# Optimization experiments

Hardware: AMD Instinct MI355X
Metric: run time of the kernel (lower is better)

## Reference

```python
import jax, jax.numpy as jnp
import numpy as np

N, C_IN, C_OUT, T, V, K = 32, 64, 128, 300, 25, 3
EPS = 1e-5


def setup_inputs() -> dict:
    key = jax.random.key(0)
    ks = jax.random.split(key, 10)
    x = jax.random.normal(ks[0], (N, C_IN, T, V), dtype=jnp.float32)
    # fixed adjacency buffer (requires_grad=False in torch) and learned attention mask
    A = jax.random.uniform(ks[1], (K, V, V), dtype=jnp.float32)
    graph_attn = jnp.ones((K, V, V), dtype=jnp.float32)  # nn.init.constant_(1)
    # per-subset 1x1 conv weights/biases, stacked: [K, C_out, C_in]
    Wg = jax.random.normal(ks[2], (K, C_OUT, C_IN), dtype=jnp.float32) * np.sqrt(2.0 / (C_OUT * K))
    bg = jnp.zeros((K, C_OUT), dtype=jnp.float32)
    # main BN affine (torch init: weight=1e-6, bias=0; use small random for a nontrivial test)
    bn_gamma = jax.random.normal(ks[3], (C_OUT,), dtype=jnp.float32) * 0.1 + 1.0
    bn_beta = jax.random.normal(ks[4], (C_OUT,), dtype=jnp.float32) * 0.1
    # residual branch (in != out): 1x1 conv + BN
    Wr = jax.random.normal(ks[5], (C_OUT, C_IN), dtype=jnp.float32) * np.sqrt(2.0 / C_IN)
    br = jnp.zeros((C_OUT,), dtype=jnp.float32)
    rbn_gamma = jax.random.normal(ks[6], (C_OUT,), dtype=jnp.float32) * 0.1 + 1.0
    rbn_beta = jax.random.normal(ks[7], (C_OUT,), dtype=jnp.float32) * 0.1
    return {"x": x, "A": A, "graph_attn": graph_attn, "Wg": Wg, "bg": bg,
            "bn_gamma": bn_gamma, "bn_beta": bn_beta,
            "Wr": Wr, "br": br, "rbn_gamma": rbn_gamma, "rbn_beta": rbn_beta}


def _batchnorm(z, gamma, beta):
    # training-mode BatchNorm2d: biased batch stats over (N, T, V)
    mean = jnp.mean(z, axis=(0, 2, 3), keepdims=True)
    var = jnp.var(z, axis=(0, 2, 3), keepdims=True)
    zhat = (z - mean) * jax.lax.rsqrt(var + EPS)
    return zhat * gamma[None, :, None, None] + beta[None, :, None, None]


def reference(x, A, graph_attn, Wg, bg, bn_gamma, bn_beta, Wr, br, rbn_gamma, rbn_beta):
    Ae = A * graph_attn                                   # [K, V, V]
    # per-subset graph aggregation: (x.view(N, C*T, V) @ Ae[k])  -> [K, N, C, T, V]
    xA = jnp.einsum('nctv,kvw->knctw', x, Ae)
    # per-subset 1x1 conv then sum over subsets; biases sum as well
    hidden = jnp.einsum('knctv,koc->notv', xA, Wg) + jnp.sum(bg, axis=0)[None, :, None, None]
    hidden = _batchnorm(hidden, bn_gamma, bn_beta)
    # residual: 1x1 conv + BN (since in_channels != out_channels)
    res = jnp.einsum('nctv,oc->notv', x, Wr) + br[None, :, None, None]
    res = _batchnorm(res, rbn_gamma, rbn_beta)
    return hidden + res
```

## Files before the change

kernel.cpp:

```cpp
#include <hip/hip_runtime.h>

typedef __attribute__((ext_vector_type(8))) _Float16 half8;
typedef __attribute__((ext_vector_type(4))) _Float16 half4v;
typedef __attribute__((ext_vector_type(4))) float float4v;
typedef __attribute__((ext_vector_type(4))) unsigned int uint4v;
typedef float float4u __attribute__((ext_vector_type(4), aligned(4)));
typedef unsigned long long u64;
typedef unsigned int u32;

#define NB   32
#define CIN  64
#define COUT 128
#define TT   300
#define VV   25
#define EPS  1e-5f
#define M_TOT 240000.0f
#define NBLK 1600
#define NTILE 4800

#define WS_WF    0
#define WS_AEF   65536
#define WS_ST    73728
#define WS_CF    75776
#define WS_WF2   77312
#define WS_TRASH 143360
#define WS_HR    1048576
#define WS_PARTP (WS_HR + 137625600)
#define WS_NEED  (WS_PARTP + 3276800)

__device__ __forceinline__ void bar_lds() {
    __builtin_amdgcn_sched_barrier(0);
    asm volatile("s_waitcnt lgkmcnt(0)" ::: "memory");
    __builtin_amdgcn_s_barrier();
    __builtin_amdgcn_sched_barrier(0);
}

__device__ __forceinline__ unsigned short f2h(float f) {
    return __builtin_bit_cast(unsigned short, (_Float16)f);
}
__device__ __forceinline__ float4v mfma16(half8 a, half8 b, float4v c) {
    return __builtin_amdgcn_mfma_f32_16x16x32_f16(a, b, c, 0, 0, 0);
}
__device__ __forceinline__ u32 pk2(float a, float b) {
    return __builtin_bit_cast(u32, __builtin_amdgcn_cvt_pkrtz(a, b));
}
__device__ __forceinline__ int hr_off(int cm, int on) {
    return (cm & 1) ? (2048 + (cm >> 1) * 768 + on * 384)
                    : ((cm >> 1) * 1024 + on * 512);
}

__global__ void prep_kernel(const float* __restrict__ A, const float* __restrict__ ga,
                            const float* __restrict__ Wg, const float* __restrict__ Wr,
                            char* __restrict__ wsb) {
    unsigned short* wf = (unsigned short*)(wsb + WS_WF);
    unsigned short* ae = (unsigned short*)(wsb + WS_AEF);
    float* st = (float*)(wsb + WS_ST);
    int i = blockIdx.x * blockDim.x + threadIdx.x;
    for (; i < 32768 + 4096 + 512; i += gridDim.x * blockDim.x) {
        if (i < 32768) {
            int on = i >> 12, kt = (i >> 9) & 7, l = (i >> 3) & 63, j = i & 7;
            int o = on * 16 + (l & 15);
            int kc = kt * 32 + ((l >> 4) << 3) + j;
            float v = (kc < 192) ? Wg[((kc >> 6) * COUT + o) * CIN + (kc & 63)]
                                 : Wr[o * CIN + (kc - 192)];
            wf[i] = f2h(v);
        } else if (i < 32768 + 4096) {
            int q = i - 32768;
            int k = q >> 10, nt = (q >> 9) & 1, l = (q >> 3) & 63, j = q & 7;
            int v = ((l >> 4) << 3) + j, w = nt * 16 + (l & 15);
            float val = 0.0f;
            if (v < VV && w < VV)
                val = (k < 3) ? A[(k * VV + v) * VV + w] * ga[(k * VV + v) * VV + w]
                              : (v == w ? 1.0f : 0.0f);
            ae[q] = f2h(val);
        } else {
            st[i - 36864] = 0.0f;
        }
    }
}

__global__ __launch_bounds__(256) void red_kernel(const float* __restrict__ part,
                                                  char* __restrict__ wsb) {
    float* st = (float*)(wsb + WS_ST);
    __shared__ float red[4][4];
    const int tid = threadIdx.x, wv = tid >> 6, lane = tid & 63;
    const int i0 = blockIdx.x * 4;
    const int bi = tid >> 2, ii = tid & 3;
    float s = 0.0f;
    for (int b = bi; b < NBLK; b += 64)
        s += part[(size_t)b * 512 + i0 + ii];
    s += __shfl_xor(s, 4);
    s += __shfl_xor(s, 8);
    s += __shfl_xor(s, 16);
    s += __shfl_xor(s, 32);
    if (lane < 4) red[wv][lane] = s;
    __syncthreads();
    if (tid < 4) st[i0 + tid] = red[0][tid] + red[1][tid] + red[2][tid] + red[3][tid];
}

__global__ __launch_bounds__(256) void scale_kernel(
        const float* __restrict__ Wg, const float* __restrict__ Wr,
        const float* __restrict__ g1, const float* __restrict__ b1,
        const float* __restrict__ g2, const float* __restrict__ b2,
        char* __restrict__ wsb, int fillw2) {
    const float* st = (const float*)(wsb + WS_ST);
    float* cf = (float*)(wsb + WS_CF);
    unsigned short* wf2 = (unsigned short*)(wsb + WS_WF2);
    __shared__ float cl[384];
    int tid = threadIdx.x;
    if (tid < 128) {
        int o = tid;
        const float inv_m = 1.0f / M_TOT;
        float mH = st[o] * inv_m,        vH = st[128 + o] * inv_m - mH * mH;
        float mR = st[256 + o] * inv_m,  vR = st[384 + o] * inv_m - mR * mR;
        float scH = g1[o] * rsqrtf(vH + EPS);
        float scR = g2[o] * rsqrtf(vR + EPS);
        float bC  = b1[o] + b2[o] - scH * mH - scR * mR;
        cl[o] = scH; cl[128 + o] = scR; cl[256 + o] = bC;
        if (blockIdx.x == 0) { cf[o] = scH; cf[128 + o] = scR; cf[256 + o] = bC; }
    }
    __syncthreads();
    if (!fillw2) return;
    for (int i = blockIdx.x * 256 + tid; i < 32768; i += gridDim.x * 256) {
        int on = i >> 12, kt = (i >> 9) & 7, l = (i >> 3) & 63, j = i & 7;
        int o = on * 16 + (l & 15);
        int kc = kt * 32 + ((l >> 4) << 3) + j;
        float v = (kc < 192) ? Wg[((kc >> 6) * COUT + o) * CIN + (kc & 63)] * cl[o]
                             : Wr[o * CIN + (kc - 192)] * cl[128 + o];
        wf2[i] = f2h(v);
    }
}

template <int MODE>
__global__ __launch_bounds__(256, 2) void gcn_kernel(
        const float* __restrict__ x, char* __restrict__ wsb, float* __restrict__ out,
        float* __restrict__ part) {
    __shared__ __align__(16) _Float16 xa[64 * 256];
    char* xab = (char*)xa;

    const unsigned short* wf = (const unsigned short*)(wsb + (MODE == 1 ? WS_WF2 : WS_WF));
    const unsigned short* ae = (const unsigned short*)(wsb + WS_AEF);
    const float* cf = (const float*)(wsb + WS_CF);

    const int tid = threadIdx.x, wv = tid >> 6, l = tid & 63;
    const int l15 = l & 15, lq = l >> 4;

    half8 af[2][8];
#pragma unroll
    for (int on = 0; on < 2; ++on)
#pragma unroll
        for (int kt = 0; kt < 8; ++kt)
            af[on][kt] = *(const half8*)&wf[(((wv * 2 + on) * 8 + kt) * 64 + l) * 8];

    half8 aef[4][2];
#pragma unroll
    for (int k = 0; k < 4; ++k)
#pragma unroll
        for (int nt = 0; nt < 2; ++nt)
            aef[k][nt] = *(const half8*)&ae[((k * 2 + nt) * 64 + l) * 8];

    float bC2[2];
    if (MODE == 1) {
#pragma unroll
        for (int on = 0; on < 2; ++on)
            bC2[on] = cf[256 + wv * 32 + on * 16 + l15];
    }

    float sH[2], sH2[2], sR[2], sR2[2];
    if (MODE != 1) {
#pragma unroll
        for (int on = 0; on < 2; ++on) { sH[on] = 0; sH2[on] = 0; sR[on] = 0; sR2[on] = 0; }
    }

    const int cRow = wv * 16 + l15;
    const int va = (lq * 8 > 16) ? 16 : lq * 8;
    float4u A1[2], A2[2];
    float Bv[2];
    auto ld_tile = [&](int n_, int t0_) {
#pragma unroll
        for (int t = 0; t < 2; ++t) {
            const float* base = x + n_ * 480000 + cRow * 7500 + (t0_ + t) * 25;
            A1[t] = *(const float4u*)(base + va);
            A2[t] = *(const float4u*)(base + va + 4);
            Bv[t] = base[24];
        }
    };
    auto mk_xf = [&](int t) -> half8 {
        u32 w0 = pk2(A1[t][0], A1[t][1]), w1 = pk2(A1[t][2], A1[t][3]);
        u32 w2 = pk2(A2[t][0], A2[t][1]), w3 = pk2(A2[t][2], A2[t][3]);
        if (lq == 3) { w0 = pk2(Bv[t], 0.0f); w1 = 0; w2 = 0; w3 = 0; }
        uint4v uw = {w0, w1, w2, w3};
        return __builtin_bit_cast(half8, uw);
    };

    const int swb = (blockIdx.x & 7) * (NBLK / 8) + (blockIdx.x >> 3);
    const int tile0 = swb * 3;
    ld_tile(tile0 / 150, (tile0 % 150) * 2);

    for (int it = 0; it < 3; ++it) {
        const int tile = tile0 + it;
        const int n = tile / 150, t0 = (tile % 150) * 2;
        bar_lds();

        half8 xf0 = mk_xf(0);
        half8 xf1 = mk_xf(1);
        if (it < 2) { int tl = tile + 1; ld_tile(tl / 150, (tl % 150) * 2); }

        {
            half8 xfs[2] = {xf0, xf1};
#pragma unroll
            for (int t = 0; t < 2; ++t)
#pragma unroll
                for (int k = 0; k < 4; ++k)
#pragma unroll
                    for (int nt = 0; nt < 2; ++nt) {
                        float4v c4 = {0.0f, 0.0f, 0.0f, 0.0f};
                        c4 = mfma16(xfs[t], aef[k][nt], c4);
                        int col = t * 32 + nt * 16 + l15;
                        int kcb = (k * 64 + wv * 16 + lq * 4) * 2;
                        u64 pk = ((u64)pk2(c4[2], c4[3]) << 32) | pk2(c4[0], c4[1]);
                        *(u64*)(xab + ((col << 9) + (kcb ^ ((col & 7) << 4)))) = pk;
                    }
        }
        bar_lds();

        char* hrw = wsb + WS_HR + (size_t)tile * 28672 + wv * 7168;

        float4v acc[4][2];
        if (MODE != 1) {
#pragma unroll
            for (int cm = 0; cm < 4; ++cm)
#pragma unroll
                for (int on = 0; on < 2; ++on) acc[cm][on] = {0.0f, 0.0f, 0.0f, 0.0f};
            __builtin_amdgcn_s_setprio(1);
#pragma unroll
            for (int kt = 0; kt < 6; ++kt)
#pragma unroll
                for (int cm = 0; cm < 4; ++cm) {
                    int col = cm * 16 + l15;
                    half8 bf = *(const half8*)(xab + ((col << 9) +
                                   ((kt * 64 + lq * 16) ^ ((col & 7) << 4))));
                    acc[cm][0] = mfma16(bf, af[0][kt], acc[cm][0]);
                    acc[cm][1] = mfma16(bf, af[1][kt], acc[cm][1]);
                }
            __builtin_amdgcn_s_setprio(0);
#pragma unroll
            for (int cm = 0; cm < 4; ++cm)
#pragma unroll
                for (int on = 0; on < 2; ++on) {
#pragma unroll
                    for (int r = 0; r < 4; ++r) {
                        float h = acc[cm][on][r];
                        sH[on] += h; sH2[on] += h * h;
                    }
                    if (MODE == 2) {
                        u64 p = (u64)pk2(acc[cm][on][0], acc[cm][on][1]) |
                                ((u64)pk2(acc[cm][on][2], acc[cm][on][3]) << 32);
                        char* dst = hrw + hr_off(cm, on) + l * 8;
                        if ((cm & 1) && lq == 3) dst = wsb + WS_TRASH;
                        *(u64*)dst = p;
                    }
                    acc[cm][on] = {0.0f, 0.0f, 0.0f, 0.0f};
                }
            __builtin_amdgcn_s_setprio(1);
#pragma unroll
            for (int kt = 6; kt < 8; ++kt)
#pragma unroll
                for (int cm = 0; cm < 4; ++cm) {
                    int col = cm * 16 + l15;
                    half8 bf = *(const half8*)(xab + ((col << 9) +
                                   ((kt * 64 + lq * 16) ^ ((col & 7) << 4))));
                    acc[cm][0] = mfma16(bf, af[0][kt], acc[cm][0]);
                    acc[cm][1] = mfma16(bf, af[1][kt], acc[cm][1]);
                }
            __builtin_amdgcn_s_setprio(0);
#pragma unroll
            for (int cm = 0; cm < 4; ++cm)
#pragma unroll
                for (int on = 0; on < 2; ++on) {
#pragma unroll
                    for (int r = 0; r < 4; ++r) {
                        float rv = acc[cm][on][r];
                        sR[on] += rv; sR2[on] += rv * rv;
                    }
                    if (MODE == 2) {
                        u64 p = (u64)pk2(acc[cm][on][0], acc[cm][on][1]) |
                                ((u64)pk2(acc[cm][on][2], acc[cm][on][3]) << 32);
                        char* dst = hrw + 3584 + hr_off(cm, on) + l * 8;
                        if ((cm & 1) && lq == 3) dst = wsb + WS_TRASH;
                        *(u64*)dst = p;
                    }
                }
        } else {
#pragma unroll
            for (int cm = 0; cm < 4; ++cm)
#pragma unroll
                for (int on = 0; on < 2; ++on)
#pragma unroll
                    for (int r = 0; r < 4; ++r) acc[cm][on][r] = bC2[on];
            __builtin_amdgcn_s_setprio(1);
#pragma unroll
            for (int kt = 0; kt < 8; ++kt)
#pragma unroll
                for (int cm = 0; cm < 4; ++cm) {
                    int col = cm * 16 + l15;
                    half8 bf = *(const half8*)(xab + ((col << 9) +
                                   ((kt * 64 + lq * 16) ^ ((col & 7) << 4))));
                    acc[cm][0] = mfma16(bf, af[0][kt], acc[cm][0]);
                    acc[cm][1] = mfma16(bf, af[1][kt], acc[cm][1]);
                }
            __builtin_amdgcn_s_setprio(0);
#pragma unroll
            for (int cm = 0; cm < 4; ++cm) {
                int t = t0 + (cm >> 1);
#pragma unroll
                for (int on = 0; on < 2; ++on) {
                    int o = wv * 32 + on * 16 + l15;
                    float* op = out + ((size_t)(n * COUT + o) * TT + t) * VV;
                    if (!(cm & 1)) {
                        *(float4u*)(op + lq * 4) = acc[cm][on];
                    } else if (lq < 2) {
                        *(float4u*)(op + 16 + lq * 4) = acc[cm][on];
                    } else if (lq == 2) {
                        op[24] = acc[cm][on][0];
                    }
                }
            }
        }
    }

    if (MODE != 1) {
#pragma unroll
        for (int on = 0; on < 2; ++on) {
            sH[on]  += __shfl_xor(sH[on], 16);  sH[on]  += __shfl_xor(sH[on], 32);
            sH2[on] += __shfl_xor(sH2[on], 16); sH2[on] += __shfl_xor(sH2[on], 32);
            sR[on]  += __shfl_xor(sR[on], 16);  sR[on]  += __shfl_xor(sR[on], 32);
            sR2[on] += __shfl_xor(sR2[on], 16); sR2[on] += __shfl_xor(sR2[on], 32);
        }
        if (l < 16) {
            float* pb = part + (size_t)blockIdx.x * 512;
#pragma unroll
            for (int on = 0; on < 2; ++on) {
                int o = wv * 32 + on * 16 + l15;
                pb[o]       = sH[on];
                pb[128 + o] = sH2[on];
                pb[256 + o] = sR[on];
                pb[384 + o] = sR2[on];
            }
        }
    }
}

__global__ __launch_bounds__(256) void bn_apply(const char* __restrict__ wsb,
                                                float* __restrict__ out) {
    __shared__ u64 lds[3584];
    const float* cf = (const float*)(wsb + WS_CF);
    const int tile = blockIdx.x;
    const int n = tile / 150, t0 = (tile % 150) * 2;
    const int tid = threadIdx.x;

    const u64* src = (const u64*)(wsb + WS_HR + (size_t)tile * 28672);
#pragma unroll
    for (int i = 0; i < 14; ++i) lds[tid + i * 256] = src[tid + i * 256];
    __syncthreads();

#pragma unroll
    for (int i = 0; i < 7; ++i) {
        int j2 = tid + i * 256;
        int row = j2 / 7, q = j2 - row * 7;
        int o = row >> 1, t = row & 1;
        int v0 = (q < 6) ? q * 4 : 24;
        int cm = t * 2 + (v0 >> 4);
        int lq = (v0 & 15) >> 2;
        int ll = lq * 16 + (o & 15);
        int wv = o >> 5, on = (o >> 4) & 1;
        int offq = (cm & 1) ? (256 + (cm >> 1) * 96 + on * 48)
                            : ((cm >> 1) * 128 + on * 64);
        u64 h64 = lds[wv * 896 + offq + ll];
        u64 r64 = lds[wv * 896 + 448 + offq + ll];
        half4v h4 = __builtin_bit_cast(half4v, h64);
        half4v r4 = __builtin_bit_cast(half4v, r64);
        float scH = cf[o], scR = cf[128 + o], bC = cf[256 + o];
        float* op = out + ((size_t)(n * COUT + o) * TT + t0 + t) * VV + v0;
        if (q < 6) {
            float4u v;
#pragma unroll
            for (int k = 0; k < 4; ++k)
                v[k] = scH * (float)h4[k] + scR * (float)r4[k] + bC;
            *(float4u*)op = v;
        } else {
            op[0] = scH * (float)h4[0] + scR * (float)r4[0] + bC;
        }
    }
}

extern "C" void kernel_launch(void* const* d_in, const int* in_sizes, int n_in,
                              void* d_out, int out_size, void* d_ws, size_t ws_size,
                              hipStream_t stream) {
    const float* x        = (const float*)d_in[0];
    const float* A        = (const float*)d_in[1];
    const float* ga       = (const float*)d_in[2];
    const float* Wg       = (const float*)d_in[3];
    const float* bn_gamma = (const float*)d_in[5];
    const float* bn_beta  = (const float*)d_in[6];
    const float* Wr       = (const float*)d_in[7];
    const float* rbn_g    = (const float*)d_in[9];
    const float* rbn_b    = (const float*)d_in[10];
    char* wsb  = (char*)d_ws;
    float* out = (float*)d_out;

    const bool primary = ws_size >= (size_t)WS_NEED + 4096;
    float* partP = (float*)(wsb + WS_PARTP);
    float* partF = (float*)(wsb + WS_HR);

    prep_kernel<<<64, 256, 0, stream>>>(A, ga, Wg, Wr, wsb);
    if (primary) {
        gcn_kernel<2><<<NBLK, 256, 0, stream>>>(x, wsb, nullptr, partP);
        red_kernel<<<128, 256, 0, stream>>>(partP, wsb);
        scale_kernel<<<64, 256, 0, stream>>>(Wg, Wr, bn_gamma, bn_beta, rbn_g, rbn_b, wsb, 0);
        bn_apply<<<NTILE, 256, 0, stream>>>(wsb, out);
    } else {
        gcn_kernel<0><<<NBLK, 256, 0, stream>>>(x, wsb, nullptr, partF);
        red_kernel<<<128, 256, 0, stream>>>(partF, wsb);
        scale_kernel<<<64, 256, 0, stream>>>(Wg, Wr, bn_gamma, bn_beta, rbn_g, rbn_b, wsb, 1);
        gcn_kernel<1><<<NBLK, 256, 0, stream>>>(x, wsb, out, partF);
    }
}
```

Before: 131.2 us.

## Double-buffer LDS stage-1 tile to overlap with stage-2 MFMA

Doubles the LDS buffer so the graph-aggregation MFMA for the next tile writes into the alternate buffer while the current tile's 1x1-conv MFMA reads the other one. This removes one barrier per iteration and lets stage 1 and stage 2 interleave. It also drops the separate scalar tail load by reading an overlapping float4 at offset 21, removes the s_setprio hints, and fully unrolls the 3-iteration loop. The cost is doubled LDS (64KB per block), which may limit occupancy at 2 blocks/CU, plus more registers for the two staged input sets.

```diff
diff --git a/kernel.cpp b/kernel.cpp
--- a/kernel.cpp
+++ b/kernel.cpp
@@ -135,7 +135,7 @@
 __global__ __launch_bounds__(256, 2) void gcn_kernel(
         const float* __restrict__ x, char* __restrict__ wsb, float* __restrict__ out,
         float* __restrict__ part) {
-    __shared__ __align__(16) _Float16 xa[64 * 256];
+    __shared__ __align__(16) _Float16 xa[2][64 * 256];
     char* xab = (char*)xa;
 
     const unsigned short* wf = (const unsigned short*)(wsb + (MODE == 1 ? WS_WF2 : WS_WF));
@@ -173,57 +173,63 @@
     }
 
     const int cRow = wv * 16 + l15;
-    const int va = (lq * 8 > 16) ? 16 : lq * 8;
-    float4u A1[2], A2[2];
-    float Bv[2];
-    auto ld_tile = [&](int n_, int t0_) {
+    const int va1 = (lq >= 2) ? 16 : lq * 8;
+    const int va2 = (lq == 3) ? 21 : va1 + 4;
+    float4u A1[2][2], A2[2][2];
+
+    auto ld_tile = [&](int s, int tl) {
+        int n_ = tl / 150, t0_ = (tl % 150) * 2;
 #pragma unroll
         for (int t = 0; t < 2; ++t) {
             const float* base = x + n_ * 480000 + cRow * 7500 + (t0_ + t) * 25;
-            A1[t] = *(const float4u*)(base + va);
-            A2[t] = *(const float4u*)(base + va + 4);
-            Bv[t] = base[24];
+            A1[s][t] = *(const float4u*)(base + va1);
+            A2[s][t] = *(const float4u*)(base + va2);
         }
     };
-    auto mk_xf = [&](int t) -> half8 {
-        u32 w0 = pk2(A1[t][0], A1[t][1]), w1 = pk2(A1[t][2], A1[t][3]);
-        u32 w2 = pk2(A2[t][0], A2[t][1]), w3 = pk2(A2[t][2], A2[t][3]);
-        if (lq == 3) { w0 = pk2(Bv[t], 0.0f); w1 = 0; w2 = 0; w3 = 0; }
+    auto mk_xf = [&](int s, int t) -> half8 {
+        u32 w0 = pk2(A1[s][t][0], A1[s][t][1]), w1 = pk2(A1[s][t][2], A1[s][t][3]);
+        u32 w2 = pk2(A2[s][t][0], A2[s][t][1]), w3 = pk2(A2[s][t][2], A2[s][t][3]);
+        if (lq == 3) { w0 = pk2(A2[s][t][3], 0.0f); w1 = 0; w2 = 0; w3 = 0; }
         uint4v uw = {w0, w1, w2, w3};
         return __builtin_bit_cast(half8, uw);
     };
+    auto do_stage1 = [&](int s, int buf) {
+        char* xb = xab + buf * 32768;
+#pragma unroll
+        for (int t = 0; t < 2; ++t) {
+            half8 xf = mk_xf(s, t);
+#pragma unroll
+            for (int k = 0; k < 4; ++k)
+#pragma unroll
+                for (int nt = 0; nt < 2; ++nt) {
+                    float4v c4 = {0.0f, 0.0f, 0.0f, 0.0f};
+                    c4 = mfma16(xf, aef[k][nt], c4);
+                    int col = t * 32 + nt * 16 + l15;
+                    int kcb = (k * 64 + wv * 16 + lq * 4) * 2;
+                    u64 pk = ((u64)pk2(c4[2], c4[3]) << 32) | pk2(c4[0], c4[1]);
+                    *(u64*)(xb + ((col << 9) + (kcb ^ ((col & 7) << 4)))) = pk;
+                }
+        }
+    };
 
     const int swb = (blockIdx.x & 7) * (NBLK / 8) + (blockIdx.x >> 3);
     const int tile0 = swb * 3;
-    ld_tile(tile0 / 150, (tile0 % 150) * 2);
-
+
+    ld_tile(0, tile0);
+    do_stage1(0, 0);
+    ld_tile(1, tile0 + 1);
+
+#pragma unroll
     for (int it = 0; it < 3; ++it) {
         const int tile = tile0 + it;
         const int n = tile / 150, t0 = (tile % 150) * 2;
+        const int buf = it & 1;
         bar_lds();
 
-        half8 xf0 = mk_xf(0);
-        half8 xf1 = mk_xf(1);
-        if (it < 2) { int tl = tile + 1; ld_tile(tl / 150, (tl % 150) * 2); }
-
-        {
-            half8 xfs[2] = {xf0, xf1};
-#pragma unroll
-            for (int t = 0; t < 2; ++t)
-#pragma unroll
-                for (int k = 0; k < 4; ++k)
-#pragma unroll
-                    for (int nt = 0; nt < 2; ++nt) {
-                        float4v c4 = {0.0f, 0.0f, 0.0f, 0.0f};
-                        c4 = mfma16(xfs[t], aef[k][nt], c4);
-                        int col = t * 32 + nt * 16 + l15;
-                        int kcb = (k * 64 + wv * 16 + lq * 4) * 2;
-                        u64 pk = ((u64)pk2(c4[2], c4[3]) << 32) | pk2(c4[0], c4[1]);
-                        *(u64*)(xab + ((col << 9) + (kcb ^ ((col & 7) << 4)))) = pk;
-                    }
-        }
-        bar_lds();
-
+        if (it == 0) ld_tile(0, tile0 + 2);
+        if (it < 2) do_stage1((it + 1) & 1, (it + 1) & 1);
+
+        char* xb = xab + buf * 32768;
         char* hrw = wsb + WS_HR + (size_t)tile * 28672 + wv * 7168;
 
         float4v acc[4][2];
@@ -232,18 +238,16 @@
             for (int cm = 0; cm < 4; ++cm)
 #pragma unroll
                 for (int on = 0; on < 2; ++on) acc[cm][on] = {0.0f, 0.0f, 0.0f, 0.0f};
-            __builtin_amdgcn_s_setprio(1);
 #pragma unroll
             for (int kt = 0; kt < 6; ++kt)
 #pragma unroll
                 for (int cm = 0; cm < 4; ++cm) {
                     int col = cm * 16 + l15;
-                    half8 bf = *(const half8*)(xab + ((col << 9) +
+                    half8 bf = *(const half8*)(xb + ((col << 9) +
                                    ((kt * 64 + lq * 16) ^ ((col & 7) << 4))));
                     acc[cm][0] = mfma16(bf, af[0][kt], acc[cm][0]);
                     acc[cm][1] = mfma16(bf, af[1][kt], acc[cm][1]);
                 }
-            __builtin_amdgcn_s_setprio(0);
 #pragma unroll
             for (int cm = 0; cm < 4; ++cm)
 #pragma unroll
@@ -262,18 +266,16 @@
                     }
                     acc[cm][on] = {0.0f, 0.0f, 0.0f, 0.0f};
                 }
-            __builtin_amdgcn_s_setprio(1);
 #pragma unroll
             for (int kt = 6; kt < 8; ++kt)
 #pragma unroll
                 for (int cm = 0; cm < 4; ++cm) {
                     int col = cm * 16 + l15;
-                    half8 bf = *(const half8*)(xab + ((col << 9) +
+                    half8 bf = *(const half8*)(xb + ((col << 9) +
                                    ((kt * 64 + lq * 16) ^ ((col & 7) << 4))));
                     acc[cm][0] = mfma16(bf, af[0][kt], acc[cm][0]);
                     acc[cm][1] = mfma16(bf, af[1][kt], acc[cm][1]);
                 }
-            __builtin_amdgcn_s_setprio(0);
 #pragma unroll
             for (int cm = 0; cm < 4; ++cm)
 #pragma unroll
@@ -298,18 +300,16 @@
                 for (int on = 0; on < 2; ++on)
 #pragma unroll
                     for (int r = 0; r < 4; ++r) acc[cm][on][r] = bC2[on];
-            __builtin_amdgcn_s_setprio(1);
 #pragma unroll
             for (int kt = 0; kt < 8; ++kt)
 #pragma unroll
                 for (int cm = 0; cm < 4; ++cm) {
                     int col = cm * 16 + l15;
-                    half8 bf = *(const half8*)(xab + ((col << 9) +
+                    half8 bf = *(const half8*)(xb + ((col << 9) +
                                    ((kt * 64 + lq * 16) ^ ((col & 7) << 4))));
                     acc[cm][0] = mfma16(bf, af[0][kt], acc[cm][0]);
                     acc[cm][1] = mfma16(bf, af[1][kt], acc[cm][1]);
                 }
-            __builtin_amdgcn_s_setprio(0);
 #pragma unroll
             for (int cm = 0; cm < 4; ++cm) {
                 int t = t0 + (cm >> 1);
```

New measurement: 123.1 us. -6.2%, faster.

## Split gcn_kernel work across 8 waves with 512-thread blocks

Applied to the files above, without the earlier changes.

Doubles the block size of gcn_kernel from 256 to 512 threads, so each wave now handles one 16-row output group instead of two, and one time step of the graph aggregation instead of two. Per-thread register arrays (weight fragments, accumulators, BN partial sums) are halved. The aim is more waves in flight to hide memory and LDS latency, and lower register pressure per thread. In exchange, each weight/B fragment loaded from LDS is reused by half as many MFMAs, and launch bounds now demand 4 blocks of 512 threads per CU.

```diff
diff --git a/kernel.cpp b/kernel.cpp
--- a/kernel.cpp
+++ b/kernel.cpp
@@ -58,8 +58,8 @@
     int i = blockIdx.x * blockDim.x + threadIdx.x;
     for (; i < 32768 + 4096 + 512; i += gridDim.x * blockDim.x) {
         if (i < 32768) {
-            int on = i >> 12, kt = (i >> 9) & 7, l = (i >> 3) & 63, j = i & 7;
-            int o = on * 16 + (l & 15);
+            int og = i >> 12, kt = (i >> 9) & 7, l = (i >> 3) & 63, j = i & 7;
+            int o = og * 16 + (l & 15);
             int kc = kt * 32 + ((l >> 4) << 3) + j;
             float v = (kc < 192) ? Wg[((kc >> 6) * COUT + o) * CIN + (kc & 63)]
                                  : Wr[o * CIN + (kc - 192)];
@@ -122,8 +122,8 @@
     __syncthreads();
     if (!fillw2) return;
     for (int i = blockIdx.x * 256 + tid; i < 32768; i += gridDim.x * 256) {
-        int on = i >> 12, kt = (i >> 9) & 7, l = (i >> 3) & 63, j = i & 7;
-        int o = on * 16 + (l & 15);
+        int og = i >> 12, kt = (i >> 9) & 7, l = (i >> 3) & 63, j = i & 7;
+        int o = og * 16 + (l & 15);
         int kc = kt * 32 + ((l >> 4) << 3) + j;
         float v = (kc < 192) ? Wg[((kc >> 6) * COUT + o) * CIN + (kc & 63)] * cl[o]
                              : Wr[o * CIN + (kc - 192)] * cl[128 + o];
@@ -132,7 +132,7 @@
 }
 
 template <int MODE>
-__global__ __launch_bounds__(256, 2) void gcn_kernel(
+__global__ __launch_bounds__(512, 4) void gcn_kernel(
         const float* __restrict__ x, char* __restrict__ wsb, float* __restrict__ out,
         float* __restrict__ part) {
     __shared__ __align__(16) _Float16 xa[64 * 256];
@@ -142,15 +142,14 @@
     const unsigned short* ae = (const unsigned short*)(wsb + WS_AEF);
     const float* cf = (const float*)(wsb + WS_CF);
 
-    const int tid = threadIdx.x, wv = tid >> 6, l = tid & 63;
+    const int tid = threadIdx.x, w = tid >> 6, l = tid & 63;
     const int l15 = l & 15, lq = l >> 4;
-
-    half8 af[2][8];
-#pragma unroll
-    for (int on = 0; on < 2; ++on)
-#pragma unroll
-        for (int kt = 0; kt < 8; ++kt)
-            af[on][kt] = *(const half8*)&wf[(((wv * 2 + on) * 8 + kt) * 64 + l) * 8];
+    const int wv4 = w & 3, tloc = w >> 2;
+
+    half8 af[8];
+#pragma unroll
+    for (int kt = 0; kt < 8; ++kt)
+        af[kt] = *(const half8*)&wf[((w * 8 + kt) * 64 + l) * 8];
 
     half8 aef[4][2];
 #pragma unroll
@@ -159,79 +158,62 @@
         for (int nt = 0; nt < 2; ++nt)
             aef[k][nt] = *(const half8*)&ae[((k * 2 + nt) * 64 + l) * 8];
 
-    float bC2[2];
-    if (MODE == 1) {
-#pragma unroll
-        for (int on = 0; on < 2; ++on)
-            bC2[on] = cf[256 + wv * 32 + on * 16 + l15];
-    }
-
-    float sH[2], sH2[2], sR[2], sR2[2];
-    if (MODE != 1) {
-#pragma unroll
-        for (int on = 0; on < 2; ++on) { sH[on] = 0; sH2[on] = 0; sR[on] = 0; sR2[on] = 0; }
-    }
-
-    const int cRow = wv * 16 + l15;
+    float bC2;
+    if (MODE == 1) bC2 = cf[256 + w * 16 + l15];
+
+    float sH = 0, sH2 = 0, sR = 0, sR2 = 0;
+
+    const int cRow = wv4 * 16 + l15;
     const int va = (lq * 8 > 16) ? 16 : lq * 8;
-    float4u A1[2], A2[2];
-    float Bv[2];
-    auto ld_tile = [&](int n_, int t0_) {
-#pragma unroll
-        for (int t = 0; t < 2; ++t) {
-            const float* base = x + n_ * 480000 + cRow * 7500 + (t0_ + t) * 25;
-            A1[t] = *(const float4u*)(base + va);
-            A2[t] = *(const float4u*)(base + va + 4);
-            Bv[t] = base[24];
-        }
+    float4u A1, A2;
+    float Bv;
+    auto ld_tile = [&](int tl) {
+        int n_ = tl / 150, t0_ = (tl % 150) * 2;
+        const float* base = x + n_ * 480000 + cRow * 7500 + (t0_ + tloc) * 25;
+        A1 = *(const float4u*)(base + va);
+        A2 = *(const float4u*)(base + va + 4);
+        Bv = base[24];
     };
-    auto mk_xf = [&](int t) -> half8 {
-        u32 w0 = pk2(A1[t][0], A1[t][1]), w1 = pk2(A1[t][2], A1[t][3]);
-        u32 w2 = pk2(A2[t][0], A2[t][1]), w3 = pk2(A2[t][2], A2[t][3]);
-        if (lq == 3) { w0 = pk2(Bv[t], 0.0f); w1 = 0; w2 = 0; w3 = 0; }
+    auto mk_xf = [&]() -> half8 {
+        u32 w0 = pk2(A1[0], A1[1]), w1 = pk2(A1[2], A1[3]);
+        u32 w2 = pk2(A2[0], A2[1]), w3 = pk2(A2[2], A2[3]);
+        if (lq == 3) { w0 = pk2(Bv, 0.0f); w1 = 0; w2 = 0; w3 = 0; }
         uint4v uw = {w0, w1, w2, w3};
         return __builtin_bit_cast(half8, uw);
     };
 
     const int swb = (blockIdx.x & 7) * (NBLK / 8) + (blockIdx.x >> 3);
     const int tile0 = swb * 3;
-    ld_tile(tile0 / 150, (tile0 % 150) * 2);
+    ld_tile(tile0);
 
     for (int it = 0; it < 3; ++it) {
         const int tile = tile0 + it;
         const int n = tile / 150, t0 = (tile % 150) * 2;
         bar_lds();
 
-        half8 xf0 = mk_xf(0);
-        half8 xf1 = mk_xf(1);
-        if (it < 2) { int tl = tile + 1; ld_tile(tl / 150, (tl % 150) * 2); }
-
-        {
-            half8 xfs[2] = {xf0, xf1};
-#pragma unroll
-            for (int t = 0; t < 2; ++t)
-#pragma unroll
-                for (int k = 0; k < 4; ++k)
-#pragma unroll
-                    for (int nt = 0; nt < 2; ++nt) {
-                        float4v c4 = {0.0f, 0.0f, 0.0f, 0.0f};
-                        c4 = mfma16(xfs[t], aef[k][nt], c4);
-                        int col = t * 32 + nt * 16 + l15;
-                        int kcb = (k * 64 + wv * 16 + lq * 4) * 2;
-                        u64 pk = ((u64)pk2(c4[2], c4[3]) << 32) | pk2(c4[0], c4[1]);
-                        *(u64*)(xab + ((col << 9) + (kcb ^ ((col & 7) << 4)))) = pk;
-                    }
-        }
+        half8 xf = mk_xf();
+        if (it < 2) ld_tile(tile + 1);
+
+#pragma unroll
+        for (int k = 0; k < 4; ++k)
+#pragma unroll
+            for (int nt = 0; nt < 2; ++nt) {
+                float4v c4 = {0.0f, 0.0f, 0.0f, 0.0f};
+                c4 = mfma16(xf, aef[k][nt], c4);
+                int col = tloc * 32 + nt * 16 + l15;
+                int kcb = (k * 64 + wv4 * 16 + lq * 4) * 2;
+                u64 pk = ((u64)pk2(c4[2], c4[3]) << 32) | pk2(c4[0], c4[1]);
+                *(u64*)(xab + ((col << 9) + (kcb ^ ((col & 7) << 4)))) = pk;
+            }
         bar_lds();
 
-        char* hrw = wsb + WS_HR + (size_t)tile * 28672 + wv * 7168;
-
-        float4v acc[4][2];
+        char* hrw = wsb + WS_HR + (size_t)tile * 28672 + (w >> 1) * 7168;
+        const int on = w & 1;
+
+        float4v acc[4];
         if (MODE != 1) {
 #pragma unroll
-            for (int cm = 0; cm < 4; ++cm)
-#pragma unroll
-                for (int on = 0; on < 2; ++on) acc[cm][on] = {0.0f, 0.0f, 0.0f, 0.0f};
+            for (int cm = 0; cm < 4; ++cm) acc[cm] = {0.0f, 0.0f, 0.0f, 0.0f};
             __builtin_amdgcn_s_setprio(1);
 #pragma unroll
             for (int kt = 0; kt < 6; ++kt)
@@ -240,28 +222,25 @@
                     int col = cm * 16 + l15;
                     half8 bf = *(const half8*)(xab + ((col << 9) +
                                    ((kt * 64 + lq * 16) ^ ((col & 7) << 4))));
-                    acc[cm][0] = mfma16(bf, af[0][kt], acc[cm][0]);
-                    acc[cm][1] = mfma16(bf, af[1][kt], acc[cm][1]);
+                    acc[cm] = mfma16(bf, af[kt], acc[cm]);
                 }
             __builtin_amdgcn_s_setprio(0);
 #pragma unroll
-            for (int cm = 0; cm < 4; ++cm)
-#pragma unroll
-                for (int on = 0; on < 2; ++on) {
-#pragma unroll
-                    for (int r = 0; r < 4; ++r) {
-                        float h = acc[cm][on][r];
-                        sH[on] += h; sH2[on] += h * h;
-                    }
-                    if (MODE == 2) {
-                        u64 p = (u64)pk2(acc[cm][on][0], acc[cm][on][1]) |
-                                ((u64)pk2(acc[cm][on][2], acc[cm][on][3]) << 32);
-                        char* dst = hrw + hr_off(cm, on) + l * 8;
-                        if ((cm & 1) && lq == 3) dst = wsb + WS_TRASH;
-                        *(u64*)dst = p;
-                    }
-                    acc[cm][on] = {0.0f, 0.0f, 0.0f, 0.0f};
-                }
+            for (int cm = 0; cm < 4; ++cm) {
+#pragma unroll
+                for (int r = 0; r < 4; ++r) {
+                    float h = acc[cm][r];
+                    sH += h; sH2 += h * h;
+                }
+                if (MODE == 2) {
+                    u64 p = (u64)pk2(acc[cm][0], acc[cm][1]) |
+                            ((u64)pk2(acc[cm][2], acc[cm][3]) << 32);
+                    char* dst = hrw + hr_off(cm, on) + l * 8;
+                    if ((cm & 1) && lq == 3) dst = wsb + WS_TRASH;
+                    *(u64*)dst = p;
+                }
+                acc[cm] = {0.0f, 0.0f, 0.0f, 0.0f};
+            }
             __builtin_amdgcn_s_setprio(1);
 #pragma unroll
             for (int kt = 6; kt < 8; ++kt)
@@ -270,34 +249,29 @@
                     int col = cm * 16 + l15;
                     half8 bf = *(const half8*)(xab + ((col << 9) +
                                    ((kt * 64 + lq * 16) ^ ((col & 7) << 4))));
-                    acc[cm][0] = mfma16(bf, af[0][kt], acc[cm][0]);
-                    acc[cm][1] = mfma16(bf, af[1][kt], acc[cm][1]);
+                    acc[cm] = mfma16(bf, af[kt], acc[cm]);
                 }
             __builtin_amdgcn_s_setprio(0);
 #pragma unroll
+            for (int cm = 0; cm < 4; ++cm) {
+#pragma unroll
+                for (int r = 0; r < 4; ++r) {
+                    float rv = acc[cm][r];
+                    sR += rv; sR2 += rv * rv;
+                }
+                if (MODE == 2) {
+                    u64 p = (u64)pk2(acc[cm][0], acc[cm][1]) |
+                            ((u64)pk2(acc[cm][2], acc[cm][3]) << 32);
+                    char* dst = hrw + 3584 + hr_off(cm, on) + l * 8;
+                    if ((cm & 1) && lq == 3) dst = wsb + WS_TRASH;
+                    *(u64*)dst = p;
+                }
+            }
+        } else {
+#pragma unroll
             for (int cm = 0; cm < 4; ++cm)
 #pragma unroll
-                for (int on = 0; on < 2; ++on) {
-#pragma unroll
-                    for (int r = 0; r < 4; ++r) {
-                        float rv = acc[cm][on][r];
-                        sR[on] += rv; sR2[on] += rv * rv;
-                    }
-                    if (MODE == 2) {
-                        u64 p = (u64)pk2(acc[cm][on][0], acc[cm][on][1]) |
-                                ((u64)pk2(acc[cm][on][2], acc[cm][on][3]) << 32);
-                        char* dst = hrw + 3584 + hr_off(cm, on) + l * 8;
-                        if ((cm & 1) && lq == 3) dst = wsb + WS_TRASH;
-                        *(u64*)dst = p;
-                    }
-                }
-        } else {
-#pragma unroll
-            for (int cm = 0; cm < 4; ++cm)
-#pragma unroll
-                for (int on = 0; on < 2; ++on)
-#pragma unroll
-                    for (int r = 0; r < 4; ++r) acc[cm][on][r] = bC2[on];
+                for (int r = 0; r < 4; ++r) acc[cm][r] = bC2;
             __builtin_amdgcn_s_setprio(1);
 #pragma unroll
             for (int kt = 0; kt < 8; ++kt)
@@ -306,47 +280,37 @@
                     int col = cm * 16 + l15;
                     half8 bf = *(const half8*)(xab + ((col << 9) +
                                    ((kt * 64 + lq * 16) ^ ((col & 7) << 4))));
-                    acc[cm][0] = mfma16(bf, af[0][kt], acc[cm][0]);
-                    acc[cm][1] = mfma16(bf, af[1][kt], acc[cm][1]);
+                    acc[cm] = mfma16(bf, af[kt], acc[cm]);
                 }
             __builtin_amdgcn_s_setprio(0);
 #pragma unroll
             for (int cm = 0; cm < 4; ++cm) {
                 int t = t0 + (cm >> 1);
-#pragma unroll
-                for (int on = 0; on < 2; ++on) {
-                    int o = wv * 32 + on * 16 + l15;
-                    float* op = out + ((size_t)(n * COUT + o) * TT + t) * VV;
-                    if (!(cm & 1)) {
-                        *(float4u*)(op + lq * 4) = acc[cm][on];
-                    } else if (lq < 2) {
-                        *(float4u*)(op + 16 + lq * 4) = acc[cm][on];
-                    } else if (lq == 2) {
-                        op[24] = acc[cm][on][0];
-                    }
+                int o = w * 16 + l15;
+                float* op = out + ((size_t)(n * COUT + o) * TT + t) * VV;
+                if (!(cm & 1)) {
+                    *(float4u*)(op + lq * 4) = acc[cm];
+                } else if (lq < 2) {
+                    *(float4u*)(op + 16 + lq * 4) = acc[cm];
+                } else if (lq == 2) {
+                    op[24] = acc[cm][0];
                 }
             }
         }
     }
 
     if (MODE != 1) {
-#pragma unroll
-        for (int on = 0; on < 2; ++on) {
-            sH[on]  += __shfl_xor(sH[on], 16);  sH[on]  += __shfl_xor(sH[on], 32);
-            sH2[on] += __shfl_xor(sH2[on], 16); sH2[on] += __shfl_xor(sH2[on], 32);
-            sR[on]  += __shfl_xor(sR[on], 16);  sR[on]  += __shfl_xor(sR[on], 32);
-            sR2[on] += __shfl_xor(sR2[on], 16); sR2[on] += __shfl_xor(sR2[on], 32);
-        }
+        sH  += __shfl_xor(sH, 16);  sH  += __shfl_xor(sH, 32);
+        sH2 += __shfl_xor(sH2, 16); sH2 += __shfl_xor(sH2, 32);
+        sR  += __shfl_xor(sR, 16);  sR  += __shfl_xor(sR, 32);
+        sR2 += __shfl_xor(sR2, 16); sR2 += __shfl_xor(sR2, 32);
         if (l < 16) {
             float* pb = part + (size_t)blockIdx.x * 512;
-#pragma unroll
-            for (int on = 0; on < 2; ++on) {
-                int o = wv * 32 + on * 16 + l15;
-                pb[o]       = sH[on];
-                pb[128 + o] = sH2[on];
-                pb[256 + o] = sR[on];
-                pb[384 + o] = sR2[on];
-            }
+            int o = w * 16 + l15;
+            pb[o]       = sH;
+            pb[128 + o] = sH2;
+            pb[256 + o] = sR;
+            pb[384 + o] = sR2;
         }
     }
 }
@@ -415,14 +379,14 @@
 
     prep_kernel<<<64, 256, 0, stream>>>(A, ga, Wg, Wr, wsb);
     if (primary) {
-        gcn_kernel<2><<<NBLK, 256, 0, stream>>>(x, wsb, nullptr, partP);
+        gcn_kernel<2><<<NBLK, 512, 0, stream>>>(x, wsb, nullptr, partP);
         red_kernel<<<128, 256, 0, stream>>>(partP, wsb);
         scale_kernel<<<64, 256, 0, stream>>>(Wg, Wr, bn_gamma, bn_beta, rbn_g, rbn_b, wsb, 0);
         bn_apply<<<NTILE, 256, 0, stream>>>(wsb, out);
     } else {
-        gcn_kernel<0><<<NBLK, 256, 0, stream>>>(x, wsb, nullptr, partF);
+        gcn_kernel<0><<<NBLK, 512, 0, stream>>>(x, wsb, nullptr, partF);
         red_kernel<<<128, 256, 0, stream>>>(partF, wsb);
         scale_kernel<<<64, 256, 0, stream>>>(Wg, Wr, bn_gamma, bn_beta, rbn_g, rbn_b, wsb, 1);
-        gcn_kernel<1><<<NBLK, 256, 0, stream>>>(x, wsb, out, partF);
-    }
-}
+        gcn_kernel<1><<<NBLK, 512, 0, stream>>>(x, wsb, out, partF);
+    }
+}
```

Result: slower. 225.8 us (+72.0%).
